# Kernel optimization log

Measured on AMD Instinct MI355X. Metric: run time of the kernel, lower is better.

Reference implementation:

```python
import jax, jax.numpy as jnp
import numpy as np

SIGMAS = (1.0, 10.0, 100.0, 1000.0)
EPS_RATIO = 1e-3  # lambda ridge term and ratio clip epsilon


def euclidsq(x, y):
    # squared pairwise Euclidean distances, [m, n]
    d = jnp.sum(x * x, axis=-1)[:, None] + jnp.sum(y * y, axis=-1)[None, :] - 2.0 * (x @ y.T)
    return jnp.maximum(d, 0.0)


def kmm_ratio(Kdede, Kdenu, lam):
    # original: inv(Kdede + lam*I) @ Kdenu @ ones == solve(A, Kdenu @ ones)
    n_de = Kdede.shape[0]
    A = Kdede + lam * jnp.eye(n_de, dtype=Kdede.dtype)
    B = jnp.sum(Kdenu, axis=1, keepdims=True)  # [n_de, 1]
    return jnp.linalg.solve(A, B)


def estimate_ratio(x_de, x_nu):
    # averaged KMM ratio over Gaussian kernels with fixed sigmas, then clip
    dsq_dede = euclidsq(x_de, x_de)
    dsq_denu = euclidsq(x_de, x_nu)
    ratio = 0.0
    for s in SIGMAS:
        inv2s2 = 1.0 / (2.0 * s * s)
        Kdede = jnp.exp(-dsq_dede * inv2s2)
        Kdenu = jnp.exp(-dsq_denu * inv2s2)
        ratio = ratio + kmm_ratio(Kdede, Kdenu, EPS_RATIO)
    ratio = ratio / len(SIGMAS)
    return jax.nn.relu(ratio) + EPS_RATIO  # clip_ratio=True


def reference(z1, z2, perm1, perm2):
    n, d = z1.shape
    z1s, z2s = z1[perm1], z2[perm2]
    # numerator ratio over full concatenated embeddings
    num_ratio = estimate_ratio(jnp.concatenate([z1, z2], axis=-1),
                               jnp.concatenate([z1s, z2s], axis=-1))
    num_ratio = 1.0 / num_ratio  # [n, 1]
    x_nu = jnp.concatenate([z2, z2], axis=-1)  # constant across samples

    def per_sample(z1_i):
        # x_de row j = concat(z1_i, z2_shuffled[j])
        x_de = jnp.concatenate([jnp.broadcast_to(z1_i, (n, d)), z2s], axis=-1)
        return jnp.sum(estimate_ratio(x_de, x_nu))

    denum_sums = jax.vmap(per_sample)(z1)  # [n]
    loss = jnp.sum(-jnp.log(num_ratio[:, 0] / denum_sums))
    return loss


def setup_inputs() -> dict:
    key = jax.random.key(0)
    k1, k2 = jax.random.split(key)
    n, d = 256, 128
    z1 = jax.random.normal(k1, (n, d), dtype=jnp.float32)
    z2 = jax.random.normal(k2, (n, d), dtype=jnp.float32)
    perm1 = jnp.arange(n, dtype=jnp.int32)
    perm2 = jnp.arange(n, dtype=jnp.int32)
    return {"z1": z1, "z2": z2, "perm1": perm1, "perm2": perm2}
```

## Files before the change

kernel.cpp:

```cpp
#include <hip/hip_runtime.h>
#include <math.h>

#define N 256
#define Dd 128

__device__ __forceinline__ double inv2s2_of(int s){
    return (s==0)?0.5:(s==1)?5.0e-3:(s==2)?5.0e-5:5.0e-7;
}

__device__ __forceinline__ void sweep32(double P[32][33], int tid){
    if (tid < 64){
        int r = tid & 31, cg = tid >> 5;
        for (int j = 0; j < 32; j++){
            double d    = P[j][j];
            double invd = 1.0 / d;
            double cr   = P[r][j];
            double s    = cr * invd;
            bool rj = (r == j);
            double nv[16];
            #pragma unroll
            for (int c = 0; c < 16; c++){
                int col = cg*16 + c;
                double pj = P[j][col];
                double v  = P[r][col];
                nv[c] = rj ? ((col == j) ? -invd : v * invd)
                           : ((col == j) ? s : v - s*pj);
            }
            #pragma unroll
            for (int c = 0; c < 16; c++) P[r][cg*16+c] = nv[c];
        }
        #pragma unroll
        for (int c = 0; c < 16; c++) P[r][cg*16+c] = -P[r][cg*16+c];
    }
}

__global__ void k_dist(const float* __restrict__ z1, const float* __restrict__ z2,
                       const int* __restrict__ p1, const int* __restrict__ p2,
                       double* __restrict__ S0, float* __restrict__ M4,
                       float* __restrict__ U4, double* __restrict__ bpart){
    __shared__ float Xs[16][17], Ys[16][17];
    int w = blockIdx.z;
    int tx = threadIdx.x, ty = threadIdx.y;
    int row = blockIdx.y*16 + ty, col = blockIdx.x*16 + tx;
    const float *Xb[2], *Yb[2]; const int *Xp[2], *Yp[2]; int npair = 1;
    Xb[1]=0; Yb[1]=0; Xp[0]=0; Yp[0]=0; Xp[1]=0; Yp[1]=0;
    switch(w){
        case 0: Xb[0]=z1; Yb[0]=z1; Xb[1]=z2; Yb[1]=z2; npair=2; break;
        case 1: Xb[0]=z1; Yb[0]=z1; Yp[0]=p1; Xb[1]=z2; Yb[1]=z2; Yp[1]=p2; npair=2; break;
        case 2: Xb[0]=z2; Yb[0]=z2; Xp[0]=p2; Yp[0]=p2; break;
        case 3: Xb[0]=z2; Yb[0]=z2; Xp[0]=p2; break;
        default:Xb[0]=z1; Yb[0]=z2; break;
    }
    double acc = 0.0;
    for (int p = 0; p < npair; p++){
        const float* X = Xb[p]; const float* Y = Yb[p];
        int xr = blockIdx.y*16 + ty; if (Xp[p]) xr = Xp[p][xr];
        int yr = blockIdx.x*16 + ty; if (Yp[p]) yr = Yp[p][yr];
        for (int c = 0; c < Dd; c += 16){
            __syncthreads();
            Xs[ty][tx] = X[xr*Dd + c + tx];
            Ys[ty][tx] = Y[yr*Dd + c + tx];
            __syncthreads();
            #pragma unroll
            for (int t = 0; t < 16; t++){
                float d = Xs[ty][t] - Ys[tx][t];
                acc += (double)d * (double)d;
            }
        }
    }
    int o = row*N + col;
    if (w == 0){
        #pragma unroll
        for (int s = 0; s < 4; s++){
            double v = exp(-inv2s2_of(s)*acc);
            if (row == col) v += 1.0e-3;
            S0[(size_t)(4+s)*N*N + o] = v;
        }
    } else if (w == 1){
        #pragma unroll
        for (int s = 0; s < 4; s++){
            double v = exp(-inv2s2_of(s)*acc);
            v += __shfl_down(v, 8, 16);
            v += __shfl_down(v, 4, 16);
            v += __shfl_down(v, 2, 16);
            v += __shfl_down(v, 1, 16);
            if (tx == 0) bpart[((size_t)s*N + row)*16 + blockIdx.x] = v;
        }
    } else if (w == 2){
        #pragma unroll
        for (int s = 0; s < 4; s++){
            double v = exp(-inv2s2_of(s)*acc);
            if (row == col) v += 1.0e-3;
            S0[(size_t)s*N*N + o] = v;
        }
    } else if (w == 3){
        #pragma unroll
        for (int s = 0; s < 4; s++) M4[s*N*N + o] = (float)exp(-inv2s2_of(s)*acc);
    } else {
        #pragma unroll
        for (int s = 0; s < 4; s++) U4[s*N*N + o] = (float)exp(-inv2s2_of(s)*acc);
    }
}

__global__ void k_gemm_nt(const float* __restrict__ M4, const float* __restrict__ U4,
                          double* __restrict__ Bmat, const double* __restrict__ S0,
                          double* __restrict__ Pg0, double* __restrict__ dsum){
    __shared__ float Ms[32][33], Us[32][33];
    __shared__ double P[32][33];
    int tx = threadIdx.x, ty = threadIdx.y;
    int tid = ty*16 + tx;
    if (blockIdx.z == 4){
        if (blockIdx.y != 0) return;
        int mat = blockIdx.x;
        if (mat == 0) dsum[tid] = 0.0;
        const double* S = S0 + (size_t)mat*65536;
        #pragma unroll
        for (int l = 0; l < 4; l++){
            int e = tid + l*256; P[e>>5][e&31] = S[(size_t)(e>>5)*N + (e&31)];
        }
        __syncthreads();
        sweep32(P, tid);
        __syncthreads();
        double* Pp = Pg0 + (size_t)mat*1024;
        #pragma unroll
        for (int l = 0; l < 4; l++){
            int e = tid + l*256; Pp[e] = P[e>>5][e&31];
        }
        return;
    }
    int s = blockIdx.z;
    const float* Mp = M4 + s*N*N;
    const float* Up = U4 + s*N*N;
    double* Bp = Bmat + s*N*N;
    int bj = blockIdx.y*32, bi = blockIdx.x*32;
    double a00=0, a01=0, a10=0, a11=0;
    for (int kc = 0; kc < N; kc += 32){
        __syncthreads();
        #pragma unroll
        for (int l = 0; l < 4; l++){
            int e = tid + l*256; int r = e >> 5, c = e & 31;
            Ms[r][c] = Mp[(bj+r)*N + kc + c];
            Us[r][c] = Up[(bi+r)*N + kc + c];
        }
        __syncthreads();
        #pragma unroll
        for (int k = 0; k < 32; k++){
            float x0 = Ms[2*ty][k], x1 = Ms[2*ty+1][k];
            float y0 = Us[2*tx][k], y1 = Us[2*tx+1][k];
            a00 += (double)x0*y0; a01 += (double)x0*y1;
            a10 += (double)x1*y0; a11 += (double)x1*y1;
        }
    }
    Bp[(bj+2*ty  )*N + bi+2*tx  ] = a00;
    Bp[(bj+2*ty  )*N + bi+2*tx+1] = a01;
    Bp[(bj+2*ty+1)*N + bi+2*tx  ] = a10;
    Bp[(bj+2*ty+1)*N + bi+2*tx+1] = a11;
}

__global__ void k_step(const double* __restrict__ Ssrc, double* __restrict__ Sdst,
                       const double* __restrict__ PgS, double* __restrict__ PgD, int k){
    __shared__ double Pl[32][33], EJ[32][33], Cl[32][33], El[32][33];
    int bx = blockIdx.x, mat = blockIdx.y;
    const double* S = Ssrc + (size_t)mat*65536;
    double* D = Sdst + (size_t)mat*65536;
    const double* Pp = PgS + (size_t)mat*1024;
    int tid = threadIdx.x;
    int Kb = k*32;
    #pragma unroll
    for (int l = 0; l < 4; l++){
        int e = tid + l*256; Pl[e>>5][e&31] = Pp[e];
    }
    if (bx < 49){
        int I = bx / 7, J = bx % 7;
        int GI = ((I < k) ? I : I + 1) * 32;
        int GJ = ((J < k) ? J : J + 1) * 32;
        #pragma unroll
        for (int l = 0; l < 4; l++){
            int e = tid + l*256; int r = e >> 5, c = e & 31;
            El[r][c] = S[(size_t)(GI + r)*N + Kb + c];
            EJ[r][c] = S[(size_t)(GJ + r)*N + Kb + c];
        }
        __syncthreads();
        #pragma unroll
        for (int l = 0; l < 4; l++){
            int e = tid + l*256; int r = e >> 5, c = e & 31;
            double acc = 0.0;
            #pragma unroll
            for (int kk = 0; kk < 32; kk++) acc += EJ[r][kk] * Pl[kk][c];
            Cl[r][c] = acc;
        }
        __syncthreads();
        int pr = tid >> 4, pc = tid & 15;
        int r0 = 2*pr, c0 = 2*pc;
        double a00 = S[(size_t)(GI+r0)*N + GJ+c0];
        double a01 = S[(size_t)(GI+r0)*N + GJ+c0+1];
        double a10 = S[(size_t)(GI+r0+1)*N + GJ+c0];
        double a11 = S[(size_t)(GI+r0+1)*N + GJ+c0+1];
        #pragma unroll
        for (int kk = 0; kk < 32; kk++){
            double e0 = El[r0][kk],   e1 = El[r0+1][kk];
            double b0 = Cl[c0][kk],   b1 = Cl[c0+1][kk];
            a00 -= e0*b0; a01 -= e0*b1;
            a10 -= e1*b0; a11 -= e1*b1;
        }
        double* Dp = D + (size_t)(GI + r0)*N + GJ + c0;
        Dp[0]   = a00; Dp[1]   = a01;
        Dp[N]   = a10; Dp[N+1] = a11;
        if (I == k && J == k && k < 7){
            __syncthreads();
            El[r0][c0]   = a00; El[r0][c0+1]   = a01;
            El[r0+1][c0] = a10; El[r0+1][c0+1] = a11;
            __syncthreads();
            sweep32(El, tid);
            __syncthreads();
            double* Pd = PgD + (size_t)mat*1024;
            #pragma unroll
            for (int l = 0; l < 4; l++){
                int e = tid + l*256; Pd[e] = El[e>>5][e&31];
            }
        }
    } else {
        int T = bx - 49;
        int GT = ((T < k) ? T : T + 1) * 32;
        #pragma unroll
        for (int l = 0; l < 4; l++){
            int e = tid + l*256; int r = e >> 5, c = e & 31;
            El[r][c] = S[(size_t)(GT + r)*N + Kb + c];
        }
        __syncthreads();
        #pragma unroll
        for (int l = 0; l < 4; l++){
            int e = tid + l*256; int r = e >> 5, c = e & 31;
            double acc = 0.0;
            #pragma unroll
            for (int kk = 0; kk < 32; kk++) acc += El[r][kk] * Pl[kk][c];
            Cl[r][c] = acc;
        }
        __syncthreads();
        #pragma unroll
        for (int l = 0; l < 4; l++){
            int e = tid + l*256; int r = e >> 5, c = e & 31;
            D[(size_t)(GT + r)*N + Kb + c] = Cl[r][c];
        }
        #pragma unroll
        for (int l = 0; l < 4; l++){
            int e = tid + l*256; int cc = e >> 5, rr = e & 31;
            D[(size_t)(Kb + cc)*N + GT + rr] = Cl[rr][cc];
        }
        if (T == 0){
            #pragma unroll
            for (int l = 0; l < 4; l++){
                int e = tid + l*256; int i = e >> 5, j = e & 31;
                D[(size_t)(Kb + i)*N + Kb + j] = -Pl[i][j];
            }
        }
    }
}

__global__ void k_x(const double* __restrict__ Sfin, const double* __restrict__ Bmat,
                    float* __restrict__ Xm){
    int s = blockIdx.z;
    const double* Sp = Sfin + (size_t)s*N*N;
    const double* Bp = Bmat + (size_t)s*N*N;
    float* Xp = Xm + (size_t)s*N*N;
    __shared__ double Gs[32][33], Bs[32][33];
    int tx = threadIdx.x, ty = threadIdx.y;
    int tid = ty*16 + tx;
    int bj = blockIdx.y*32, bi = blockIdx.x*32;
    double a00=0, a01=0, a10=0, a11=0;
    for (int kc = 0; kc < N; kc += 32){
        __syncthreads();
        #pragma unroll
        for (int l = 0; l < 4; l++){
            int e = tid + l*256; int r = e >> 5, c = e & 31;
            Gs[r][c] = -Sp[(size_t)(bj+r)*N + kc + c];
            Bs[r][c] = Bp[(size_t)(kc+r)*N + bi + c];
        }
        __syncthreads();
        #pragma unroll
        for (int k = 0; k < 32; k++){
            double x0 = Gs[2*ty][k], x1 = Gs[2*ty+1][k];
            double y0 = Bs[k][2*tx], y1 = Bs[k][2*tx+1];
            a00 += x0*y0; a01 += x0*y1;
            a10 += x1*y0; a11 += x1*y1;
        }
    }
    Xp[(bj+2*ty  )*N + bi+2*tx  ] = (float)a00;
    Xp[(bj+2*ty  )*N + bi+2*tx+1] = (float)a01;
    Xp[(bj+2*ty+1)*N + bi+2*tx  ] = (float)a10;
    Xp[(bj+2*ty+1)*N + bi+2*tx+1] = (float)a11;
}

__global__ void k_red(const float* __restrict__ Xm, const double* __restrict__ Sfin,
                      const double* __restrict__ bpart, double* __restrict__ dsum,
                      float* __restrict__ rnum){
    __shared__ double cp[32][33];
    __shared__ double bsh[256];
    int b = blockIdx.x, tid = threadIdx.x;
    if (b < 64){
        int bj = (b >> 3)*32, bi = (b & 7)*32;
        #pragma unroll
        for (int l = 0; l < 4; l++){
            int e = tid + l*256; int r = e >> 5, c = e & 31;
            int o = (bj + r)*N + bi + c;
            float x = Xm[0*N*N + o] + Xm[1*N*N + o] + Xm[2*N*N + o] + Xm[3*N*N + o];
            cp[r][c] = (double)fmaxf(0.25f*x, 0.f);
        }
        __syncthreads();
        if (tid < 32){
            double ssum = 0;
            #pragma unroll
            for (int r = 0; r < 32; r++) ssum += cp[r][tid];
            atomicAdd(&dsum[bi + tid], ssum);
        }
    } else {
        int s = b - 64, j = tid;
        const double* Sn = Sfin + (size_t)(4+s)*N*N;
        const double* bp = bpart + (size_t)s*N*16;
        double acc = 0;
        #pragma unroll
        for (int t = 0; t < 16; t++) acc += bp[j*16 + t];
        bsh[j] = acc;
        __syncthreads();
        double y = 0;
        for (int k = 0; k < N; k++) y -= Sn[(size_t)k*N + j] * bsh[k];
        rnum[s*N + j] = (float)y;
    }
}

__global__ void k_loss2(const double* __restrict__ dsum, const float* __restrict__ rnum,
                        float* __restrict__ out){
    __shared__ double red[256];
    int i = threadIdx.x;
    double denum = dsum[i] + (double)N * 1.0e-3;
    float ravg = 0.25f*(rnum[0*N+i] + rnum[1*N+i] + rnum[2*N+i] + rnum[3*N+i]);
    double rn = (double)fmaxf(ravg, 0.f) + 1.0e-3;
    red[i] = log(rn) + log(denum);
    __syncthreads();
    for (int st = 128; st > 0; st >>= 1){
        if (i < st) red[i] += red[i + st];
        __syncthreads();
    }
    if (i == 0) out[0] = (float)red[0];
}

extern "C" void kernel_launch(void* const* d_in, const int* in_sizes, int n_in,
                              void* d_out, int out_size, void* d_ws, size_t ws_size,
                              hipStream_t stream) {
    (void)in_sizes; (void)n_in; (void)out_size; (void)ws_size;
    const float* z1 = (const float*)d_in[0];
    const float* z2 = (const float*)d_in[1];
    const int*   p1 = (const int*)d_in[2];
    const int*   p2 = (const int*)d_in[3];
    float* out = (float*)d_out;

    char* w = (char*)d_ws;
    size_t o = 0;
    auto carve = [&](size_t bytes) -> char* {
        char* p = w + o;
        o += (bytes + 255) & ~(size_t)255;
        return p;
    };
    double* bpart = (double*)carve((size_t)4*N*16*sizeof(double));
    double* dsum  = (double*)carve((size_t)N*sizeof(double));
    float*  M4    = (float*) carve((size_t)4*N*N*sizeof(float));
    float*  U4    = (float*) carve((size_t)4*N*N*sizeof(float));
    double* Bmat  = (double*)carve((size_t)4*N*N*sizeof(double));
    float*  Xm    = (float*) carve((size_t)4*N*N*sizeof(float));
    float*  rnum  = (float*) carve((size_t)4*N*sizeof(float));
    double* S0    = (double*)carve((size_t)8*N*N*sizeof(double));
    double* S1    = (double*)carve((size_t)8*N*N*sizeof(double));
    double* Pg0   = (double*)carve((size_t)8*32*32*sizeof(double));
    double* Pg1   = (double*)carve((size_t)8*32*32*sizeof(double));

    k_dist<<<dim3(16,16,5), dim3(16,16), 0, stream>>>(z1, z2, p1, p2,
                                                      S0, M4, U4, bpart);
    k_gemm_nt<<<dim3(8,8,5), dim3(16,16), 0, stream>>>(M4, U4, Bmat, S0, Pg0, dsum);
    for (int k = 0; k < 8; k++){
        double* src = (k & 1) ? S1 : S0;
        double* dst = (k & 1) ? S0 : S1;
        double* ps  = (k & 1) ? Pg1 : Pg0;
        double* pd  = (k & 1) ? Pg0 : Pg1;
        k_step<<<dim3(56,8), dim3(256), 0, stream>>>(src, dst, ps, pd, k);
    }
    k_x<<<dim3(8,8,4), dim3(16,16), 0, stream>>>(S0, Bmat, Xm);
    k_red<<<dim3(68), dim3(256), 0, stream>>>(Xm, S0, bpart, dsum, rnum);
    k_loss2<<<dim3(1), dim3(256), 0, stream>>>(dsum, rnum, out);
}
```

Baseline: 438.8 us.

## Exploit symmetry in block sweep updates and batch global loads into registers

The blocked Gauss-Jordan sweep kernel now updates only the lower-triangular 32x32 tiles (28 instead of 49 per matrix) and writes each off-diagonal result back transposed, relying on the matrices being symmetric. Global loads of the pivot block and panels are issued into registers before the shared-memory stores, so several memory accesses are in flight at once. This cuts launched blocks and compute per step, but adds a transposed store pass with extra barriers and depends on symmetry being preserved throughout the elimination.

```diff
diff --git a/kernel.cpp b/kernel.cpp
--- a/kernel.cpp
+++ b/kernel.cpp
@@ -10,7 +10,7 @@
 
 __device__ __forceinline__ void sweep32(double P[32][33], int tid){
     if (tid < 64){
-        int r = tid & 31, cg = tid >> 5;
+        int r = tid & 31, cg_ = tid >> 5;
         for (int j = 0; j < 32; j++){
             double d    = P[j][j];
             double invd = 1.0 / d;
@@ -20,17 +20,17 @@
             double nv[16];
             #pragma unroll
             for (int c = 0; c < 16; c++){
-                int col = cg*16 + c;
+                int col = cg_*16 + c;
                 double pj = P[j][col];
                 double v  = P[r][col];
                 nv[c] = rj ? ((col == j) ? -invd : v * invd)
                            : ((col == j) ? s : v - s*pj);
             }
             #pragma unroll
-            for (int c = 0; c < 16; c++) P[r][cg*16+c] = nv[c];
-        }
-        #pragma unroll
-        for (int c = 0; c < 16; c++) P[r][cg*16+c] = -P[r][cg*16+c];
+            for (int c = 0; c < 16; c++) P[r][cg_*16+c] = nv[c];
+        }
+        #pragma unroll
+        for (int c = 0; c < 16; c++) P[r][cg_*16+c] = -P[r][cg_*16+c];
     }
 }
 
@@ -166,36 +166,42 @@
     const double* Pp = PgS + (size_t)mat*1024;
     int tid = threadIdx.x;
     int Kb = k*32;
-    #pragma unroll
-    for (int l = 0; l < 4; l++){
-        int e = tid + l*256; Pl[e>>5][e&31] = Pp[e];
-    }
-    if (bx < 49){
-        int I = bx / 7, J = bx % 7;
+    if (bx < 28){
+        int I = 0, b = bx;
+        while (b >= I+1){ b -= I+1; I++; }
+        int J = b;
         int GI = ((I < k) ? I : I + 1) * 32;
         int GJ = ((J < k) ? J : J + 1) * 32;
-        #pragma unroll
-        for (int l = 0; l < 4; l++){
-            int e = tid + l*256; int r = e >> 5, c = e & 31;
-            El[r][c] = S[(size_t)(GI + r)*N + Kb + c];
-            EJ[r][c] = S[(size_t)(GJ + r)*N + Kb + c];
-        }
-        __syncthreads();
-        #pragma unroll
-        for (int l = 0; l < 4; l++){
-            int e = tid + l*256; int r = e >> 5, c = e & 31;
-            double acc = 0.0;
-            #pragma unroll
-            for (int kk = 0; kk < 32; kk++) acc += EJ[r][kk] * Pl[kk][c];
-            Cl[r][c] = acc;
-        }
-        __syncthreads();
-        int pr = tid >> 4, pc = tid & 15;
-        int r0 = 2*pr, c0 = 2*pc;
+        int r0 = 2*(tid >> 4), c0 = 2*(tid & 15);
+        double rP[4], rE[4], rEJ[4];
+        #pragma unroll
+        for (int l = 0; l < 4; l++){
+            int e = tid + l*256; int r = e >> 5, c = e & 31;
+            rP[l]  = Pp[e];
+            rE[l]  = S[(size_t)(GI + r)*N + Kb + c];
+            rEJ[l] = S[(size_t)(GJ + r)*N + Kb + c];
+        }
         double a00 = S[(size_t)(GI+r0)*N + GJ+c0];
         double a01 = S[(size_t)(GI+r0)*N + GJ+c0+1];
         double a10 = S[(size_t)(GI+r0+1)*N + GJ+c0];
         double a11 = S[(size_t)(GI+r0+1)*N + GJ+c0+1];
+        #pragma unroll
+        for (int l = 0; l < 4; l++){
+            int e = tid + l*256; int r = e >> 5, c = e & 31;
+            Pl[r][c] = rP[l];
+            El[r][c] = rE[l];
+            EJ[r][c] = rEJ[l];
+        }
+        __syncthreads();
+        #pragma unroll
+        for (int l = 0; l < 4; l++){
+            int e = tid + l*256; int r = e >> 5, c = e & 31;
+            double acc = 0.0;
+            #pragma unroll
+            for (int kk = 0; kk < 32; kk++) acc += EJ[r][kk] * Pl[kk][c];
+            Cl[r][c] = acc;
+        }
+        __syncthreads();
         #pragma unroll
         for (int kk = 0; kk < 32; kk++){
             double e0 = El[r0][kk],   e1 = El[r0+1][kk];
@@ -206,7 +212,17 @@
         double* Dp = D + (size_t)(GI + r0)*N + GJ + c0;
         Dp[0]   = a00; Dp[1]   = a01;
         Dp[N]   = a10; Dp[N+1] = a11;
-        if (I == k && J == k && k < 7){
+        if (I != J){
+            __syncthreads();
+            EJ[r0][c0]   = a00; EJ[r0][c0+1]   = a01;
+            EJ[r0+1][c0] = a10; EJ[r0+1][c0+1] = a11;
+            __syncthreads();
+            #pragma unroll
+            for (int l = 0; l < 4; l++){
+                int e = tid + l*256; int r = e >> 5, c = e & 31;
+                D[(size_t)(GJ + r)*N + GI + c] = EJ[c][r];
+            }
+        } else if (I == k && k < 7){
             __syncthreads();
             El[r0][c0]   = a00; El[r0][c0+1]   = a01;
             El[r0+1][c0] = a10; El[r0+1][c0+1] = a11;
@@ -220,12 +236,20 @@
             }
         }
     } else {
-        int T = bx - 49;
+        int T = bx - 28;
         int GT = ((T < k) ? T : T + 1) * 32;
-        #pragma unroll
-        for (int l = 0; l < 4; l++){
-            int e = tid + l*256; int r = e >> 5, c = e & 31;
-            El[r][c] = S[(size_t)(GT + r)*N + Kb + c];
+        double rP[4], rE[4];
+        #pragma unroll
+        for (int l = 0; l < 4; l++){
+            int e = tid + l*256; int r = e >> 5, c = e & 31;
+            rP[l] = Pp[e];
+            rE[l] = S[(size_t)(GT + r)*N + Kb + c];
+        }
+        #pragma unroll
+        for (int l = 0; l < 4; l++){
+            int e = tid + l*256; int r = e >> 5, c = e & 31;
+            Pl[r][c] = rP[l];
+            El[r][c] = rE[l];
         }
         __syncthreads();
         #pragma unroll
@@ -381,7 +405,7 @@
         double* dst = (k & 1) ? S0 : S1;
         double* ps  = (k & 1) ? Pg1 : Pg0;
         double* pd  = (k & 1) ? Pg0 : Pg1;
-        k_step<<<dim3(56,8), dim3(256), 0, stream>>>(src, dst, ps, pd, k);
+        k_step<<<dim3(35,8), dim3(256), 0, stream>>>(src, dst, ps, pd, k);
     }
     k_x<<<dim3(8,8,4), dim3(16,16), 0, stream>>>(S0, Bmat, Xm);
     k_red<<<dim3(68), dim3(256), 0, stream>>>(Xm, S0, bpart, dsum, rnum);
```

After: 434.1 us (median of 2 runs). No clear change (-1.1%).

## Fuse two block-sweep pivot steps per launch using symmetric lower-triangle tiles

Applied to the files above, without the earlier changes.

Replaces the eight per-pivot block sweep launches with four launches that each eliminate two 32-wide pivot blocks. Each block recomputes the second pivot's Schur complement locally and inverts it redundantly, and only lower-triangle tiles are computed, with symmetric mirror stores. This is meant to cut launch count and global round trips of the 256x256 matrices. In exchange every block does extra redundant small GEMMs and a 32x32 sweep, and the sequence has many more __syncthreads barriers.

```diff
diff --git a/kernel.cpp b/kernel.cpp
--- a/kernel.cpp
+++ b/kernel.cpp
@@ -10,7 +10,7 @@
 
 __device__ __forceinline__ void sweep32(double P[32][33], int tid){
     if (tid < 64){
-        int r = tid & 31, cg = tid >> 5;
+        int r = tid & 31, cg_ = tid >> 5;
         for (int j = 0; j < 32; j++){
             double d    = P[j][j];
             double invd = 1.0 / d;
@@ -20,18 +20,111 @@
             double nv[16];
             #pragma unroll
             for (int c = 0; c < 16; c++){
-                int col = cg*16 + c;
+                int col = cg_*16 + c;
                 double pj = P[j][col];
                 double v  = P[r][col];
                 nv[c] = rj ? ((col == j) ? -invd : v * invd)
                            : ((col == j) ? s : v - s*pj);
             }
             #pragma unroll
-            for (int c = 0; c < 16; c++) P[r][cg*16+c] = nv[c];
-        }
-        #pragma unroll
-        for (int c = 0; c < 16; c++) P[r][cg*16+c] = -P[r][cg*16+c];
-    }
+            for (int c = 0; c < 16; c++) P[r][cg_*16+c] = nv[c];
+        }
+        #pragma unroll
+        for (int c = 0; c < 16; c++) P[r][cg_*16+c] = -P[r][cg_*16+c];
+    }
+}
+
+__device__ __forceinline__ void ld_tile(double T[32][33], const double* __restrict__ G, int tid){
+    __syncthreads();
+    #pragma unroll
+    for (int l=0;l<4;l++){ int e=tid+l*256; int r=e>>5,c=e&31; T[r][c]=G[(size_t)r*N+c]; }
+    __syncthreads();
+}
+__device__ __forceinline__ void ld_pg(double T[32][33], const double* __restrict__ P, int tid){
+    __syncthreads();
+    #pragma unroll
+    for (int l=0;l<4;l++){ int e=tid+l*256; T[e>>5][e&31]=P[e]; }
+    __syncthreads();
+}
+__device__ __forceinline__ void st_tile(double* __restrict__ G, const double T[32][33], int tid){
+    __syncthreads();
+    #pragma unroll
+    for (int l=0;l<4;l++){ int e=tid+l*256; int r=e>>5,c=e&31; G[(size_t)r*N+c]=T[r][c]; }
+}
+__device__ __forceinline__ void st_tileT(double* __restrict__ G, const double T[32][33], int tid){
+    __syncthreads();
+    #pragma unroll
+    for (int l=0;l<4;l++){ int e=tid+l*256; int r=e>>5,c=e&31; G[(size_t)r*N+c]=T[c][r]; }
+}
+__device__ __forceinline__ void mm_nn(double D[32][33], const double A[32][33],
+                                      const double B[32][33], int tid){
+    __syncthreads();
+    double acc[4];
+    #pragma unroll
+    for (int l=0;l<4;l++){ int e=tid+l*256; int r=e>>5,c=e&31; double s=0.0;
+        #pragma unroll
+        for (int kk=0;kk<32;kk++) s += A[r][kk]*B[kk][c];
+        acc[l]=s; }
+    __syncthreads();
+    #pragma unroll
+    for (int l=0;l<4;l++){ int e=tid+l*256; D[e>>5][e&31]=acc[l]; }
+    __syncthreads();
+}
+__device__ __forceinline__ void mm_nt_subG(double D[32][33], const double* __restrict__ G,
+                                           const double A[32][33], const double B[32][33], int tid){
+    __syncthreads();
+    double acc[4];
+    #pragma unroll
+    for (int l=0;l<4;l++){ int e=tid+l*256; int r=e>>5,c=e&31; double s=G[(size_t)r*N+c];
+        #pragma unroll
+        for (int kk=0;kk<32;kk++) s -= A[r][kk]*B[c][kk];
+        acc[l]=s; }
+    __syncthreads();
+    #pragma unroll
+    for (int l=0;l<4;l++){ int e=tid+l*256; D[e>>5][e&31]=acc[l]; }
+    __syncthreads();
+}
+__device__ __forceinline__ void mm_nt_subL(double D[32][33], const double A[32][33],
+                                           const double B[32][33], int tid){
+    __syncthreads();
+    double acc[4];
+    #pragma unroll
+    for (int l=0;l<4;l++){ int e=tid+l*256; int r=e>>5,c=e&31; double s=D[r][c];
+        #pragma unroll
+        for (int kk=0;kk<32;kk++) s -= A[r][kk]*B[c][kk];
+        acc[l]=s; }
+    __syncthreads();
+    #pragma unroll
+    for (int l=0;l<4;l++){ int e=tid+l*256; D[e>>5][e&31]=acc[l]; }
+    __syncthreads();
+}
+__device__ __forceinline__ void mm_nn_subL(double D[32][33], const double A[32][33],
+                                           const double B[32][33], int tid){
+    __syncthreads();
+    double acc[4];
+    #pragma unroll
+    for (int l=0;l<4;l++){ int e=tid+l*256; int r=e>>5,c=e&31; double s=D[r][c];
+        #pragma unroll
+        for (int kk=0;kk<32;kk++) s -= A[r][kk]*B[kk][c];
+        acc[l]=s; }
+    __syncthreads();
+    #pragma unroll
+    for (int l=0;l<4;l++){ int e=tid+l*256; D[e>>5][e&31]=acc[l]; }
+    __syncthreads();
+}
+__device__ __forceinline__ void mm_negtn(double D[32][33], const double P[32][33],
+                                         const double A[32][33], const double Z[32][33], int tid){
+    __syncthreads();
+    double acc[4];
+    #pragma unroll
+    for (int l=0;l<4;l++){ int e=tid+l*256; int r=e>>5,c=e&31; double s=-P[r][c];
+        #pragma unroll
+        for (int kk=0;kk<32;kk++) s -= A[kk][r]*Z[kk][c];
+        acc[l]=s; }
+    __syncthreads();
+    #pragma unroll
+    for (int l=0;l<4;l++){ int e=tid+l*256; D[e>>5][e&31]=acc[l]; }
+    __syncthreads();
 }
 
 __global__ void k_dist(const float* __restrict__ z1, const float* __restrict__ z2,
@@ -157,102 +250,76 @@
     Bp[(bj+2*ty+1)*N + bi+2*tx+1] = a11;
 }
 
-__global__ void k_step(const double* __restrict__ Ssrc, double* __restrict__ Sdst,
-                       const double* __restrict__ PgS, double* __restrict__ PgD, int k){
-    __shared__ double Pl[32][33], EJ[32][33], Cl[32][33], El[32][33];
-    int bx = blockIdx.x, mat = blockIdx.y;
+__global__ void __launch_bounds__(256) k_step2(
+    const double* __restrict__ Ssrc, double* __restrict__ Sdst,
+    const double* __restrict__ PgS, double* __restrict__ PgD, int k)
+{
+    __shared__ double T0[32][33], T1[32][33], T2[32][33], T3[32][33],
+                      T4[32][33], T5[32][33], T6[32][33];
+    int tid = threadIdx.x;
+    int mat = blockIdx.y;
     const double* S = Ssrc + (size_t)mat*65536;
     double* D = Sdst + (size_t)mat*65536;
-    const double* Pp = PgS + (size_t)mat*1024;
-    int tid = threadIdx.x;
-    int Kb = k*32;
-    #pragma unroll
-    for (int l = 0; l < 4; l++){
-        int e = tid + l*256; Pl[e>>5][e&31] = Pp[e];
-    }
-    if (bx < 49){
-        int I = bx / 7, J = bx % 7;
-        int GI = ((I < k) ? I : I + 1) * 32;
-        int GJ = ((J < k) ? J : J + 1) * 32;
-        #pragma unroll
-        for (int l = 0; l < 4; l++){
-            int e = tid + l*256; int r = e >> 5, c = e & 31;
-            El[r][c] = S[(size_t)(GI + r)*N + Kb + c];
-            EJ[r][c] = S[(size_t)(GJ + r)*N + Kb + c];
-        }
-        __syncthreads();
-        #pragma unroll
-        for (int l = 0; l < 4; l++){
-            int e = tid + l*256; int r = e >> 5, c = e & 31;
-            double acc = 0.0;
-            #pragma unroll
-            for (int kk = 0; kk < 32; kk++) acc += EJ[r][kk] * Pl[kk][c];
-            Cl[r][c] = acc;
-        }
-        __syncthreads();
-        int pr = tid >> 4, pc = tid & 15;
-        int r0 = 2*pr, c0 = 2*pc;
-        double a00 = S[(size_t)(GI+r0)*N + GJ+c0];
-        double a01 = S[(size_t)(GI+r0)*N + GJ+c0+1];
-        double a10 = S[(size_t)(GI+r0+1)*N + GJ+c0];
-        double a11 = S[(size_t)(GI+r0+1)*N + GJ+c0+1];
-        #pragma unroll
-        for (int kk = 0; kk < 32; kk++){
-            double e0 = El[r0][kk],   e1 = El[r0+1][kk];
-            double b0 = Cl[c0][kk],   b1 = Cl[c0+1][kk];
-            a00 -= e0*b0; a01 -= e0*b1;
-            a10 -= e1*b0; a11 -= e1*b1;
-        }
-        double* Dp = D + (size_t)(GI + r0)*N + GJ + c0;
-        Dp[0]   = a00; Dp[1]   = a01;
-        Dp[N]   = a10; Dp[N+1] = a11;
-        if (I == k && J == k && k < 7){
-            __syncthreads();
-            El[r0][c0]   = a00; El[r0][c0+1]   = a01;
-            El[r0+1][c0] = a10; El[r0+1][c0+1] = a11;
-            __syncthreads();
-            sweep32(El, tid);
-            __syncthreads();
+    int q = k + 1, nk = k + 2;
+    int a = 0, bb = blockIdx.x;
+    while (bb >= a+1){ bb -= a+1; a++; }
+    int b = bb;
+    auto TS = [&](int r, int c){ return S + (size_t)(r*32)*N + c*32; };
+    auto TD = [&](int r, int c){ return D + (size_t)(r*32)*N + c*32; };
+
+    ld_pg(T0, PgS + (size_t)mat*1024, tid);
+    ld_tile(T1, TS(q,k), tid);
+    mm_nn(T2, T1, T0, tid);
+    mm_nt_subG(T3, TS(q,q), T2, T1, tid);
+    __syncthreads(); sweep32(T3, tid); __syncthreads();
+
+    if (a == q && b == q){
+        __syncthreads();
+        double* G = TD(q,q);
+        #pragma unroll
+        for (int l=0;l<4;l++){ int e=tid+l*256; int r=e>>5,c=e&31; G[(size_t)r*N+c] = -T3[r][c]; }
+    } else if (a == k && b == k){
+        mm_nn(T4, T3, T2, tid);
+        mm_negtn(T5, T0, T2, T4, tid);
+        st_tile(TD(k,k), T5, tid);
+    } else if (a == q && b == k){
+        mm_nn(T4, T3, T2, tid);
+        st_tile (TD(q,k), T4, tid);
+        st_tileT(TD(k,q), T4, tid);
+    } else if (b == k || a == k){
+        int x = (b == k) ? a : b;
+        ld_tile(T4, TS(x,k), tid);
+        mm_nn(T5, T4, T0, tid);
+        mm_nt_subG(T6, TS(x,q), T5, T1, tid);
+        mm_nn(T4, T6, T3, tid);
+        mm_nn_subL(T5, T4, T2, tid);
+        st_tile (TD(x,k), T5, tid);
+        st_tileT(TD(k,x), T5, tid);
+    } else if (a == q || b == q){
+        int x = (a == q) ? b : a;
+        ld_tile(T4, TS(x,k), tid);
+        mm_nn(T5, T4, T0, tid);
+        mm_nt_subG(T6, TS(x,q), T5, T1, tid);
+        mm_nn(T4, T6, T3, tid);
+        st_tile (TD(x,q), T4, tid);
+        st_tileT(TD(q,x), T4, tid);
+    } else {
+        ld_tile(T4, TS(a,k), tid);
+        mm_nn(T5, T4, T0, tid);
+        mm_nt_subG(T2, TS(a,q), T5, T1, tid);
+        ld_tile(T4, TS(b,k), tid);
+        mm_nn(T6, T4, T0, tid);
+        mm_nt_subG(T0, TS(b,q), T6, T1, tid);
+        mm_nn(T6, T2, T3, tid);
+        mm_nt_subG(T1, TS(a,b), T5, T4, tid);
+        mm_nt_subL(T1, T6, T0, tid);
+        st_tile(TD(a,b), T1, tid);
+        if (a != b) st_tileT(TD(b,a), T1, tid);
+        if (a == nk && b == nk && k < 6){
+            __syncthreads(); sweep32(T1, tid); __syncthreads();
             double* Pd = PgD + (size_t)mat*1024;
             #pragma unroll
-            for (int l = 0; l < 4; l++){
-                int e = tid + l*256; Pd[e] = El[e>>5][e&31];
-            }
-        }
-    } else {
-        int T = bx - 49;
-        int GT = ((T < k) ? T : T + 1) * 32;
-        #pragma unroll
-        for (int l = 0; l < 4; l++){
-            int e = tid + l*256; int r = e >> 5, c = e & 31;
-            El[r][c] = S[(size_t)(GT + r)*N + Kb + c];
-        }
-        __syncthreads();
-        #pragma unroll
-        for (int l = 0; l < 4; l++){
-            int e = tid + l*256; int r = e >> 5, c = e & 31;
-            double acc = 0.0;
-            #pragma unroll
-            for (int kk = 0; kk < 32; kk++) acc += El[r][kk] * Pl[kk][c];
-            Cl[r][c] = acc;
-        }
-        __syncthreads();
-        #pragma unroll
-        for (int l = 0; l < 4; l++){
-            int e = tid + l*256; int r = e >> 5, c = e & 31;
-            D[(size_t)(GT + r)*N + Kb + c] = Cl[r][c];
-        }
-        #pragma unroll
-        for (int l = 0; l < 4; l++){
-            int e = tid + l*256; int cc = e >> 5, rr = e & 31;
-            D[(size_t)(Kb + cc)*N + GT + rr] = Cl[rr][cc];
-        }
-        if (T == 0){
-            #pragma unroll
-            for (int l = 0; l < 4; l++){
-                int e = tid + l*256; int i = e >> 5, j = e & 31;
-                D[(size_t)(Kb + i)*N + Kb + j] = -Pl[i][j];
-            }
+            for (int l=0;l<4;l++){ int e=tid+l*256; Pd[e] = T1[e>>5][e&31]; }
         }
     }
 }
@@ -376,12 +443,13 @@
     k_dist<<<dim3(16,16,5), dim3(16,16), 0, stream>>>(z1, z2, p1, p2,
                                                       S0, M4, U4, bpart);
     k_gemm_nt<<<dim3(8,8,5), dim3(16,16), 0, stream>>>(M4, U4, Bmat, S0, Pg0, dsum);
-    for (int k = 0; k < 8; k++){
-        double* src = (k & 1) ? S1 : S0;
-        double* dst = (k & 1) ? S0 : S1;
-        double* ps  = (k & 1) ? Pg1 : Pg0;
-        double* pd  = (k & 1) ? Pg0 : Pg1;
-        k_step<<<dim3(56,8), dim3(256), 0, stream>>>(src, dst, ps, pd, k);
+    for (int j = 0; j < 4; j++){
+        int k = 2*j;
+        double* src = (j & 1) ? S1 : S0;
+        double* dst = (j & 1) ? S0 : S1;
+        double* ps  = (j & 1) ? Pg1 : Pg0;
+        double* pd  = (j & 1) ? Pg0 : Pg1;
+        k_step2<<<dim3(36,8), dim3(256), 0, stream>>>(src, dst, ps, pd, k);
     }
     k_x<<<dim3(8,8,4), dim3(16,16), 0, stream>>>(S0, Bmat, Xm);
     k_red<<<dim3(68), dim3(256), 0, stream>>>(Xm, S0, bpart, dsum, rnum);
```

After: 629.1 us. 43.4% more time.
